# Optimization experiments

Hardware: AMD Instinct MI355X
Metric: run time of the kernel (lower is better)

The kernel has to match this reference:

```python
import jax, jax.numpy as jnp
import numpy as np

B, S, D, H = 2, 2048, 1024, 16
DK = D // H
NEG = -1e9
EPS = 1e-5


def setup_inputs() -> dict:
    key = jax.random.key(0)
    ks = jax.random.split(key, 6)
    sd = 0.02
    return {
        "x": jax.random.normal(ks[0], (B, S, D), jnp.float32),
        "mask": jax.random.randint(ks[1], (B, 1, S), 0, 2, jnp.int32),
        "wq": jax.random.normal(ks[2], (D, D), jnp.float32) * sd,
        "bq": jnp.zeros((D,), jnp.float32),
        "wk": jax.random.normal(ks[3], (D, D), jnp.float32) * sd,
        "bk": jnp.zeros((D,), jnp.float32),
        "wv": jax.random.normal(ks[4], (D, D), jnp.float32) * sd,
        "bv": jnp.zeros((D,), jnp.float32),
        "wf": jax.random.normal(ks[5], (D, D), jnp.float32) * sd,
        "bf": jnp.zeros((D,), jnp.float32),
        "ln_g": jnp.ones((D,), jnp.float32),
        "ln_b": jnp.zeros((D,), jnp.float32),
    }


def reference(x, mask, wq, bq, wk, bk, wv, bv, wf, bf, ln_g, ln_b):
    b, s, d = x.shape
    scale = jnp.asarray(DK ** 0.5, x.dtype)
    # QKV projections -> (b, h, s, dk)
    def split_heads(y):
        return y.reshape(b, s, H, DK).transpose(0, 2, 1, 3)
    q = split_heads(x @ wq + bq)
    k = split_heads(x @ wk + bk)
    v = split_heads(x @ wv + bv)
    # scores (b, h, s, s)
    att = jnp.einsum("bhqd,bhkd->bhqk", q / scale, k)
    m = mask[:, None, :, :]  # (b,1,1,s) broadcast over heads & queries
    att = jnp.where(m == 0, jnp.asarray(NEG, att.dtype), att)
    att = jax.nn.softmax(att, axis=-1)
    ctx = jnp.einsum("bhqk,bhkd->bhqd", att, v)
    ctx = ctx.transpose(0, 2, 1, 3).reshape(b, s, d)
    out = ctx @ wf + bf + x  # residual (dropout=0, eval)
    # LayerNorm
    mu = out.mean(-1, keepdims=True)
    var = out.var(-1, keepdims=True)
    out = (out - mu) * jax.lax.rsqrt(var + EPS) * ln_g + ln_b
    return out, att
```

## Files before the change

### kernel.cpp

```cpp
#include <hip/hip_runtime.h>

typedef unsigned short u16;
typedef unsigned int u32;
typedef unsigned long long u64;
typedef u16 u16x4 __attribute__((ext_vector_type(4)));
typedef u16 u16x8 __attribute__((ext_vector_type(8)));
typedef __bf16 bf16x8 __attribute__((ext_vector_type(8)));
typedef float f32x4 __attribute__((ext_vector_type(4)));

__device__ __forceinline__ u16 f2bf(float f) {
  u32 u = __float_as_uint(f);
  u += 0x7fffu + ((u >> 16) & 1u);
  return (u16)(u >> 16);
}

__device__ __forceinline__ f32x4 mfma16(bf16x8 a, bf16x8 b, f32x4 c) {
  return __builtin_amdgcn_mfma_f32_16x16x32_bf16(a, b, c, 0, 0, 0);
}

__device__ __forceinline__ void gload16(const void* g, void* l) {
  __builtin_amdgcn_global_load_lds(
      (const __attribute__((address_space(1))) unsigned char*)g,
      (__attribute__((address_space(3))) unsigned char*)l, 16, 0, 0);
}

__global__ __launch_bounds__(256) void cast_x_kernel(const float* __restrict__ x,
                                                     u16* __restrict__ xb) {
  int i = blockIdx.x * 256 + threadIdx.x;
  float4 v = ((const float4*)x)[i];
  u16x4 o = { f2bf(v.x), f2bf(v.y), f2bf(v.z), f2bf(v.w) };
  ((u16x4*)xb)[i] = o;
}

__global__ __launch_bounds__(256) void tcast_kernel(
    const float* __restrict__ w0, const float* __restrict__ w1,
    const float* __restrict__ w2, const float* __restrict__ w3,
    u16* __restrict__ o0, u16* __restrict__ o1, u16* __restrict__ o2, u16* __restrict__ o3) {
  const int z = blockIdx.z;
  const float* src = (z == 0) ? w0 : (z == 1) ? w1 : (z == 2) ? w2 : w3;
  u16* dst = (z == 0) ? o0 : (z == 1) ? o1 : (z == 2) ? o2 : o3;
  __shared__ u16 t[64][72];
  const int tid = threadIdx.x;
  const int n0 = blockIdx.x * 64, k0 = blockIdx.y * 64;
#pragma unroll
  for (int i = 0; i < 4; ++i) {
    int r = (tid >> 4) + i * 16;
    int c = (tid & 15) * 4;
    float4 v = *(const float4*)&src[(size_t)(k0 + r) * 1024 + n0 + c];
    t[c + 0][r] = f2bf(v.x);
    t[c + 1][r] = f2bf(v.y);
    t[c + 2][r] = f2bf(v.z);
    t[c + 3][r] = f2bf(v.w);
  }
  __syncthreads();
#pragma unroll
  for (int i = 0; i < 2; ++i) {
    int nl = (tid >> 3) + i * 32;
    int ks = (tid & 7) * 8;
    *(u16x8*)&dst[(size_t)(n0 + nl) * 1024 + k0 + ks] = *(const u16x8*)&t[nl][ks];
  }
}

__global__ __launch_bounds__(256, 2) void gemm_qkv_kernel(
    const u16* __restrict__ A,
    const u16* __restrict__ BqT, const u16* __restrict__ BkT, const u16* __restrict__ BvT,
    const float* __restrict__ bq, const float* __restrict__ bk, const float* __restrict__ bv,
    u16* __restrict__ qo, u16* __restrict__ ko, u16* __restrict__ vo) {
  const int z = blockIdx.z;
  const u16* Bt = (z == 0) ? BqT : (z == 1) ? BkT : BvT;
  const float* bias = (z == 0) ? bq : (z == 1) ? bk : bv;
  u16* outp = (z == 0) ? qo : (z == 1) ? ko : vo;
  const float osc = (z == 0) ? 0.125f : 1.0f;

  __shared__ u16 As[128][32];
  __shared__ u16 Bs[128][32];

  const int tid = threadIdx.x;
  const int lane = tid & 63, w = tid >> 6;
  const int wr = w >> 1, wc = w & 1;
  const int ln = lane & 15, quad = lane >> 4;
  const int kc = quad * 8;
  const int m0 = blockIdx.y * 128, n0 = blockIdx.x * 128;
  const int sr = w * 16 + (lane >> 2);
  const int sc = (lane & 3) * 8;

  f32x4 acc[4][4] = {};

  for (int k0 = 0; k0 < 1024; k0 += 32) {
    __syncthreads();
#pragma unroll
    for (int j = 0; j < 2; ++j) {
      gload16(&A[(size_t)(m0 + sr + j * 64) * 1024 + k0 + sc], &As[w * 16 + j * 64][0]);
      gload16(&Bt[(size_t)(n0 + sr + j * 64) * 1024 + k0 + sc], &Bs[w * 16 + j * 64][0]);
    }
    __syncthreads();
    bf16x8 af[4], bfr[4];
#pragma unroll
    for (int t = 0; t < 4; ++t) af[t] = *(const bf16x8*)&As[wr * 64 + t * 16 + ln][kc];
#pragma unroll
    for (int t = 0; t < 4; ++t) bfr[t] = *(const bf16x8*)&Bs[wc * 64 + t * 16 + ln][kc];
#pragma unroll
    for (int mt = 0; mt < 4; ++mt)
#pragma unroll
      for (int nt = 0; nt < 4; ++nt)
        acc[mt][nt] = mfma16(af[mt], bfr[nt], acc[mt][nt]);
  }

  if (z == 2) {
#pragma unroll
    for (int nt = 0; nt < 4; ++nt) {
      const int n = n0 + wc * 64 + nt * 16 + ln;
      const float bv2 = bias[n];
      const int h = n >> 6, dk = n & 63;
#pragma unroll
      for (int mt = 0; mt < 4; ++mt) {
        const int mb = m0 + wr * 64 + mt * 16 + quad * 4;
        const int b = mb >> 11, s = mb & 2047;
        u16x4 pk = { f2bf(acc[mt][nt][0] + bv2), f2bf(acc[mt][nt][1] + bv2),
                     f2bf(acc[mt][nt][2] + bv2), f2bf(acc[mt][nt][3] + bv2) };
        *(u16x4*)&outp[((size_t)((b * 16 + h) * 64 + dk)) * 2048 + s] = pk;
      }
    }
  } else {
#pragma unroll
    for (int nt = 0; nt < 4; ++nt) {
      const int n = n0 + wc * 64 + nt * 16 + ln;
      const float bv2 = bias[n];
      const int h = n >> 6, dk = n & 63;
#pragma unroll
      for (int mt = 0; mt < 4; ++mt) {
#pragma unroll
        for (int r = 0; r < 4; ++r) {
          const int m = m0 + wr * 64 + mt * 16 + quad * 4 + r;
          const int b = m >> 11, s = m & 2047;
          outp[((size_t)((b * 16 + h) * 2048 + s)) * 64 + dk] = f2bf((acc[mt][nt][r] + bv2) * osc);
        }
      }
    }
  }
}

__global__ __launch_bounds__(256, 3) void attn_kernel(
    const u16* __restrict__ q_ws, const u16* __restrict__ k_ws, const u16* __restrict__ vT,
    const int* __restrict__ mask, float* __restrict__ att, u16* __restrict__ ctx_ws) {
  __shared__ u16 Qs[64][72];
  __shared__ u16 KsF[2][64 * 64];
  __shared__ u16 VsF[2][64 * 64];
  __shared__ u16 PsF[4][16 * 64];

  const int tid = threadIdx.x, lane = tid & 63, w = tid >> 6;
  const int ln = lane & 15, quad = lane >> 4, kc = quad * 8;
  const int bh = blockIdx.y, b = bh >> 4, h = bh & 15;
  const int q0 = blockIdx.x * 64;
  const size_t base = (size_t)bh * 2048 * 64;
  const size_t vbase = (size_t)bh * 64 * 2048;

  const int rl = lane >> 3;
  const int sw16 = ((lane & 7) ^ rl) << 3;
  const int xi0 = (quad * 8) ^ ((ln & 7) << 3);
  const int xi1 = xi0 ^ 32;

  {
    int r = tid >> 2, c = (tid & 3) * 16;
    size_t g = base + (size_t)(q0 + r) * 64 + c;
    *(u16x8*)&Qs[r][c] = *(const u16x8*)&q_ws[g];
    *(u16x8*)&Qs[r][c + 8] = *(const u16x8*)&q_ws[g + 8];
  }

  const int* mrow = mask + b * 2048;
  u64 mm0 = 0, mm1 = 0;
#pragma unroll
  for (int kt = 0; kt < 16; ++kt) {
#pragma unroll
    for (int nt = 0; nt < 4; ++nt) {
      mm0 |= (u64)(mrow[kt * 64 + nt * 16 + ln] != 0) << (kt * 4 + nt);
      mm1 |= (u64)(mrow[(kt + 16) * 64 + nt * 16 + ln] != 0) << (kt * 4 + nt);
    }
  }

  {
    const int rr = w * 16;
    gload16(&k_ws[base + (size_t)(rr + rl) * 64 + sw16], &KsF[0][rr * 64]);
    gload16(&k_ws[base + (size_t)(rr + 8 + rl) * 64 + sw16], &KsF[0][(rr + 8) * 64]);
    gload16(&vT[vbase + (size_t)(rr + rl) * 2048 + sw16], &VsF[0][rr * 64]);
    gload16(&vT[vbase + (size_t)(rr + 8 + rl) * 2048 + sw16], &VsF[0][(rr + 8) * 64]);
  }
  __syncthreads();
  const bf16x8 aq0 = *(const bf16x8*)&Qs[w * 16 + ln][kc];
  const bf16x8 aq1 = *(const bf16x8*)&Qs[w * 16 + ln][kc + 32];

  float l_[4] = {0.f, 0.f, 0.f, 0.f};
  f32x4 ctx[4] = {};

  for (int kt = 0; kt < 32; ++kt) {
    const u16* Kc = KsF[kt & 1];
    const u16* Vc = VsF[kt & 1];
    if (kt < 31) {
      u16* Kn = KsF[(kt + 1) & 1];
      u16* Vn = VsF[(kt + 1) & 1];
      const int rr = w * 16;
#pragma unroll
      for (int j = 0; j < 2; ++j) {
        gload16(&k_ws[base + (size_t)((kt + 1) * 64 + rr + j * 8 + rl) * 64 + sw16],
                &Kn[(rr + j * 8) * 64]);
        gload16(&vT[vbase + (size_t)(rr + j * 8 + rl) * 2048 + (kt + 1) * 64 + sw16],
                &Vn[(rr + j * 8) * 64]);
      }
    }
    const u32 mbits = (u32)(((kt < 16) ? (mm0 >> ((kt & 15) * 4)) : (mm1 >> ((kt & 15) * 4))) & 0xf);
    f32x4 st[4];
#pragma unroll
    for (int nt = 0; nt < 4; ++nt) {
      const int row = nt * 16 + ln;
      bf16x8 b0 = *(const bf16x8*)&Kc[row * 64 + xi0];
      bf16x8 b1 = *(const bf16x8*)&Kc[row * 64 + xi1];
      f32x4 zz = {0.f, 0.f, 0.f, 0.f};
      zz = mfma16(aq0, b0, zz);
      zz = mfma16(aq1, b1, zz);
      st[nt] = zz;
    }
#pragma unroll
    for (int nt = 0; nt < 4; ++nt) {
      const float msel = (float)((mbits >> nt) & 1u);
#pragma unroll
      for (int r = 0; r < 4; ++r) {
        float p = __expf(st[nt][r]) * msel;
        st[nt][r] = p;
        const int qr = quad * 4 + r;
        PsF[w][(qr << 6) | ((nt * 16 + ln) ^ ((qr & 7) << 3))] = f2bf(p);
      }
    }
#pragma unroll
    for (int r = 0; r < 4; ++r) {
      float ss = st[0][r] + st[1][r] + st[2][r] + st[3][r];
      ss += __shfl_xor(ss, 1, 16);
      ss += __shfl_xor(ss, 2, 16);
      ss += __shfl_xor(ss, 4, 16);
      ss += __shfl_xor(ss, 8, 16);
      l_[r] += ss;
    }
    const int pr = ln * 64;
    const bf16x8 ap0 = *(const bf16x8*)&PsF[w][pr + xi0];
    const bf16x8 ap1 = *(const bf16x8*)&PsF[w][pr + xi1];
#pragma unroll
    for (int ct = 0; ct < 4; ++ct) {
      const int row = ct * 16 + ln;
      bf16x8 v0 = *(const bf16x8*)&Vc[row * 64 + xi0];
      bf16x8 v1 = *(const bf16x8*)&Vc[row * 64 + xi1];
      ctx[ct] = mfma16(ap0, v0, ctx[ct]);
      ctx[ct] = mfma16(ap1, v1, ctx[ct]);
    }
    __syncthreads();
  }

  float linv[4];
#pragma unroll
  for (int r = 0; r < 4; ++r) linv[r] = 1.0f / l_[r];
#pragma unroll
  for (int ct = 0; ct < 4; ++ct)
#pragma unroll
    for (int r = 0; r < 4; ++r) ctx[ct][r] *= linv[r];

#pragma unroll
  for (int ct = 0; ct < 4; ++ct) {
#pragma unroll
    for (int r = 0; r < 4; ++r) {
      int q = q0 + w * 16 + quad * 4 + r;
      int dk = ct * 16 + ln;
      ctx_ws[(size_t)(b * 2048 + q) * 1024 + h * 64 + dk] = f2bf(ctx[ct][r]);
    }
  }

  {
    const int rr = w * 16;
    gload16(&k_ws[base + (size_t)(rr + rl) * 64 + sw16], &KsF[0][rr * 64]);
    gload16(&k_ws[base + (size_t)(rr + 8 + rl) * 64 + sw16], &KsF[0][(rr + 8) * 64]);
  }
  __syncthreads();
  for (int kt = 0; kt < 32; ++kt) {
    const u16* Kc = KsF[kt & 1];
    if (kt < 31) {
      u16* Kn = KsF[(kt + 1) & 1];
      const int rr = w * 16;
#pragma unroll
      for (int j = 0; j < 2; ++j)
        gload16(&k_ws[base + (size_t)((kt + 1) * 64 + rr + j * 8 + rl) * 64 + sw16],
                &Kn[(rr + j * 8) * 64]);
    }
    const u32 mbits = (u32)(((kt < 16) ? (mm0 >> ((kt & 15) * 4)) : (mm1 >> ((kt & 15) * 4))) & 0xf);
    f32x4 st[4];
#pragma unroll
    for (int nt = 0; nt < 4; ++nt) {
      const int row = nt * 16 + ln;
      bf16x8 b0 = *(const bf16x8*)&Kc[row * 64 + xi0];
      bf16x8 b1 = *(const bf16x8*)&Kc[row * 64 + xi1];
      f32x4 zz = {0.f, 0.f, 0.f, 0.f};
      zz = mfma16(aq0, b0, zz);
      zz = mfma16(aq1, b1, zz);
      st[nt] = zz;
    }
#pragma unroll
    for (int nt = 0; nt < 4; ++nt) {
      const int sg = kt * 64 + nt * 16 + ln;
      const float msel = (float)((mbits >> nt) & 1u);
#pragma unroll
      for (int r = 0; r < 4; ++r) {
        float p = __expf(st[nt][r]) * linv[r] * msel;
        __builtin_nontemporal_store(
            p, &att[((size_t)bh * 2048 + q0 + w * 16 + quad * 4 + r) * 2048 + sg]);
      }
    }
    __syncthreads();
  }
}

__global__ __launch_bounds__(256, 2) void gemm_out_kernel(
    const u16* __restrict__ A, const u16* __restrict__ Bt, const float* __restrict__ bias,
    const float* __restrict__ resid, float* __restrict__ outp) {
  __shared__ u16 As[128][32];
  __shared__ u16 Bs[128][32];

  const int tid = threadIdx.x;
  const int lane = tid & 63, w = tid >> 6;
  const int wr = w >> 1, wc = w & 1;
  const int ln = lane & 15, quad = lane >> 4;
  const int kc = quad * 8;
  const int m0 = blockIdx.y * 128, n0 = blockIdx.x * 128;
  const int sr = w * 16 + (lane >> 2);
  const int sc = (lane & 3) * 8;

  f32x4 acc[4][4] = {};

  for (int k0 = 0; k0 < 1024; k0 += 32) {
    __syncthreads();
#pragma unroll
    for (int j = 0; j < 2; ++j) {
      gload16(&A[(size_t)(m0 + sr + j * 64) * 1024 + k0 + sc], &As[w * 16 + j * 64][0]);
      gload16(&Bt[(size_t)(n0 + sr + j * 64) * 1024 + k0 + sc], &Bs[w * 16 + j * 64][0]);
    }
    __syncthreads();
    bf16x8 af[4], bfr[4];
#pragma unroll
    for (int t = 0; t < 4; ++t) af[t] = *(const bf16x8*)&As[wr * 64 + t * 16 + ln][kc];
#pragma unroll
    for (int t = 0; t < 4; ++t) bfr[t] = *(const bf16x8*)&Bs[wc * 64 + t * 16 + ln][kc];
#pragma unroll
    for (int mt = 0; mt < 4; ++mt)
#pragma unroll
      for (int nt = 0; nt < 4; ++nt)
        acc[mt][nt] = mfma16(af[mt], bfr[nt], acc[mt][nt]);
  }

#pragma unroll
  for (int nt = 0; nt < 4; ++nt) {
    const int n = n0 + wc * 64 + nt * 16 + ln;
    const float bv2 = bias[n];
#pragma unroll
    for (int mt = 0; mt < 4; ++mt) {
#pragma unroll
      for (int r = 0; r < 4; ++r) {
        const int m = m0 + wr * 64 + mt * 16 + quad * 4 + r;
        outp[(size_t)m * 1024 + n] = acc[mt][nt][r] + bv2 + resid[(size_t)m * 1024 + n];
      }
    }
  }
}

__global__ __launch_bounds__(256) void ln_kernel(float* __restrict__ io,
                                                 const float* __restrict__ g,
                                                 const float* __restrict__ bta) {
  const int row = blockIdx.x, tid = threadIdx.x;
  float* p = io + (size_t)row * 1024;
  float4 v = ((const float4*)p)[tid];
  float s = v.x + v.y + v.z + v.w;
  float s2 = v.x * v.x + v.y * v.y + v.z * v.z + v.w * v.w;
#pragma unroll
  for (int off = 32; off > 0; off >>= 1) {
    s += __shfl_xor(s, off, 64);
    s2 += __shfl_xor(s2, off, 64);
  }
  __shared__ float red[8];
  const int w = tid >> 6, lane = tid & 63;
  if (lane == 0) { red[w] = s; red[4 + w] = s2; }
  __syncthreads();
  s = red[0] + red[1] + red[2] + red[3];
  s2 = red[4] + red[5] + red[6] + red[7];
  const float mu = s * (1.0f / 1024.0f);
  const float var = s2 * (1.0f / 1024.0f) - mu * mu;
  const float rs = rsqrtf(var + 1e-5f);
  float4 gg = ((const float4*)g)[tid];
  float4 bb = ((const float4*)bta)[tid];
  float4 o;
  o.x = (v.x - mu) * rs * gg.x + bb.x;
  o.y = (v.y - mu) * rs * gg.y + bb.y;
  o.z = (v.z - mu) * rs * gg.z + bb.z;
  o.w = (v.w - mu) * rs * gg.w + bb.w;
  ((float4*)p)[tid] = o;
}

extern "C" void kernel_launch(void* const* d_in, const int* in_sizes, int n_in,
                              void* d_out, int out_size, void* d_ws, size_t ws_size,
                              hipStream_t stream) {
  const float* x = (const float*)d_in[0];
  const int* mask = (const int*)d_in[1];
  const float* wq = (const float*)d_in[2];
  const float* bq = (const float*)d_in[3];
  const float* wk = (const float*)d_in[4];
  const float* bk = (const float*)d_in[5];
  const float* wv = (const float*)d_in[6];
  const float* bv = (const float*)d_in[7];
  const float* wf = (const float*)d_in[8];
  const float* bf_ = (const float*)d_in[9];
  const float* ln_g = (const float*)d_in[10];
  const float* ln_b = (const float*)d_in[11];

  float* out = (float*)d_out;
  float* att = out + (size_t)4194304;

  char* ws = (char*)d_ws;
  u16* xb   = (u16*)(ws);
  u16* wqT  = (u16*)(ws + ((size_t)8 << 20));
  u16* wkT  = (u16*)(ws + ((size_t)10 << 20));
  u16* wvT  = (u16*)(ws + ((size_t)12 << 20));
  u16* wfT  = (u16*)(ws + ((size_t)14 << 20));
  u16* q_ws = (u16*)(ws + ((size_t)16 << 20));
  u16* k_ws = (u16*)(ws + ((size_t)24 << 20));
  u16* vT   = (u16*)(ws + ((size_t)32 << 20));
  u16* ctxw = (u16*)(ws + ((size_t)40 << 20));

  cast_x_kernel<<<4096, 256, 0, stream>>>(x, xb);
  tcast_kernel<<<dim3(16, 16, 4), 256, 0, stream>>>(wq, wk, wv, wf, wqT, wkT, wvT, wfT);
  gemm_qkv_kernel<<<dim3(8, 32, 3), 256, 0, stream>>>(xb, wqT, wkT, wvT, bq, bk, bv,
                                                      q_ws, k_ws, vT);
  attn_kernel<<<dim3(32, 32), 256, 0, stream>>>(q_ws, k_ws, vT, mask, att, ctxw);
  gemm_out_kernel<<<dim3(8, 32), 256, 0, stream>>>(ctxw, wfT, bf_, x, out);
  ln_kernel<<<4096, 256, 0, stream>>>(out, ln_g, ln_b);
}
```

Baseline: 762.9 us.

## Split attention-probability store into separate kernel with vectorized transposed-MFMA writes

The second pass that recomputes QK^T and writes the full attention matrix moves out of the flash-attention kernel into its own kernel. The attention kernel now saves the per-row inverse softmax sums to a workspace buffer. The new kernel computes S^T with swapped MFMA operands, so each lane holds four consecutive keys and can issue 16-byte nontemporal float4 stores instead of scalar ones. The mask is staged as floats in LDS and Q is loaded directly into registers. The cost is an extra launch and reloading K, in exchange for coalesced writes of the 512 MB att output and lower register and LDS pressure in each kernel.

After: 836.4 us. 9.6% more time.

```diff
diff --git a/kernel.cpp b/kernel.cpp
--- a/kernel.cpp
+++ b/kernel.cpp
@@ -142,11 +142,11 @@
 
 __global__ __launch_bounds__(256, 3) void attn_kernel(
     const u16* __restrict__ q_ws, const u16* __restrict__ k_ws, const u16* __restrict__ vT,
-    const int* __restrict__ mask, float* __restrict__ att, u16* __restrict__ ctx_ws) {
-  __shared__ u16 Qs[64][72];
+    const int* __restrict__ mask, float* __restrict__ Lbuf, u16* __restrict__ ctx_ws) {
   __shared__ u16 KsF[2][64 * 64];
   __shared__ u16 VsF[2][64 * 64];
   __shared__ u16 PsF[4][16 * 64];
+  __shared__ float Ms[2048];
 
   const int tid = threadIdx.x, lane = tid & 63, w = tid >> 6;
   const int ln = lane & 15, quad = lane >> 4, kc = quad * 8;
@@ -161,22 +161,17 @@
   const int xi1 = xi0 ^ 32;
 
   {
-    int r = tid >> 2, c = (tid & 3) * 16;
-    size_t g = base + (size_t)(q0 + r) * 64 + c;
-    *(u16x8*)&Qs[r][c] = *(const u16x8*)&q_ws[g];
-    *(u16x8*)&Qs[r][c + 8] = *(const u16x8*)&q_ws[g + 8];
-  }
-
-  const int* mrow = mask + b * 2048;
-  u64 mm0 = 0, mm1 = 0;
-#pragma unroll
-  for (int kt = 0; kt < 16; ++kt) {
-#pragma unroll
-    for (int nt = 0; nt < 4; ++nt) {
-      mm0 |= (u64)(mrow[kt * 64 + nt * 16 + ln] != 0) << (kt * 4 + nt);
-      mm1 |= (u64)(mrow[(kt + 16) * 64 + nt * 16 + ln] != 0) << (kt * 4 + nt);
-    }
-  }
+    const int* mrow = mask + b * 2048;
+    int4 a0 = ((const int4*)mrow)[tid * 2];
+    int4 a1 = ((const int4*)mrow)[tid * 2 + 1];
+    float4 f0 = { a0.x ? 1.f : 0.f, a0.y ? 1.f : 0.f, a0.z ? 1.f : 0.f, a0.w ? 1.f : 0.f };
+    float4 f1 = { a1.x ? 1.f : 0.f, a1.y ? 1.f : 0.f, a1.z ? 1.f : 0.f, a1.w ? 1.f : 0.f };
+    *(float4*)&Ms[tid * 8] = f0;
+    *(float4*)&Ms[tid * 8 + 4] = f1;
+  }
+
+  const bf16x8 aq0 = *(const bf16x8*)&q_ws[base + (size_t)(q0 + w * 16 + ln) * 64 + kc];
+  const bf16x8 aq1 = *(const bf16x8*)&q_ws[base + (size_t)(q0 + w * 16 + ln) * 64 + kc + 32];
 
   {
     const int rr = w * 16;
@@ -186,8 +181,6 @@
     gload16(&vT[vbase + (size_t)(rr + 8 + rl) * 2048 + sw16], &VsF[0][(rr + 8) * 64]);
   }
   __syncthreads();
-  const bf16x8 aq0 = *(const bf16x8*)&Qs[w * 16 + ln][kc];
-  const bf16x8 aq1 = *(const bf16x8*)&Qs[w * 16 + ln][kc + 32];
 
   float l_[4] = {0.f, 0.f, 0.f, 0.f};
   f32x4 ctx[4] = {};
@@ -207,7 +200,6 @@
                 &Vn[(rr + j * 8) * 64]);
       }
     }
-    const u32 mbits = (u32)(((kt < 16) ? (mm0 >> ((kt & 15) * 4)) : (mm1 >> ((kt & 15) * 4))) & 0xf);
     f32x4 st[4];
 #pragma unroll
     for (int nt = 0; nt < 4; ++nt) {
@@ -221,7 +213,7 @@
     }
 #pragma unroll
     for (int nt = 0; nt < 4; ++nt) {
-      const float msel = (float)((mbits >> nt) & 1u);
+      const float msel = Ms[kt * 64 + nt * 16 + ln];
 #pragma unroll
       for (int r = 0; r < 4; ++r) {
         float p = __expf(st[nt][r]) * msel;
@@ -261,6 +253,11 @@
 #pragma unroll
     for (int r = 0; r < 4; ++r) ctx[ct][r] *= linv[r];
 
+  if (ln == 0) {
+#pragma unroll
+    for (int r = 0; r < 4; ++r) Lbuf[(size_t)bh * 2048 + q0 + w * 16 + quad * 4 + r] = linv[r];
+  }
+
 #pragma unroll
   for (int ct = 0; ct < 4; ++ct) {
 #pragma unroll
@@ -270,6 +267,40 @@
       ctx_ws[(size_t)(b * 2048 + q) * 1024 + h * 64 + dk] = f2bf(ctx[ct][r]);
     }
   }
+}
+
+__global__ __launch_bounds__(256, 4) void att_store_kernel(
+    const u16* __restrict__ q_ws, const u16* __restrict__ k_ws,
+    const int* __restrict__ mask, const float* __restrict__ Lbuf,
+    float* __restrict__ att) {
+  __shared__ u16 KsF[2][64 * 64];
+  __shared__ float Ms[2048];
+
+  const int tid = threadIdx.x, lane = tid & 63, w = tid >> 6;
+  const int ln = lane & 15, quad = lane >> 4, kc = quad * 8;
+  const int bh = blockIdx.y, b = bh >> 4;
+  const int q0 = blockIdx.x * 64;
+  const size_t base = (size_t)bh * 2048 * 64;
+
+  const int rl = lane >> 3;
+  const int sw16 = ((lane & 7) ^ rl) << 3;
+  const int xi0 = (quad * 8) ^ ((ln & 7) << 3);
+  const int xi1 = xi0 ^ 32;
+
+  {
+    const int* mrow = mask + b * 2048;
+    int4 a0 = ((const int4*)mrow)[tid * 2];
+    int4 a1 = ((const int4*)mrow)[tid * 2 + 1];
+    float4 f0 = { a0.x ? 1.f : 0.f, a0.y ? 1.f : 0.f, a0.z ? 1.f : 0.f, a0.w ? 1.f : 0.f };
+    float4 f1 = { a1.x ? 1.f : 0.f, a1.y ? 1.f : 0.f, a1.z ? 1.f : 0.f, a1.w ? 1.f : 0.f };
+    *(float4*)&Ms[tid * 8] = f0;
+    *(float4*)&Ms[tid * 8 + 4] = f1;
+  }
+
+  const bf16x8 aq0 = *(const bf16x8*)&q_ws[base + (size_t)(q0 + w * 16 + ln) * 64 + kc];
+  const bf16x8 aq1 = *(const bf16x8*)&q_ws[base + (size_t)(q0 + w * 16 + ln) * 64 + kc + 32];
+  const float lsv = Lbuf[(size_t)bh * 2048 + q0 + w * 16 + ln];
+  float* orow = att + ((size_t)bh * 2048 + q0 + w * 16 + ln) * 2048;
 
   {
     const int rr = w * 16;
@@ -277,6 +308,7 @@
     gload16(&k_ws[base + (size_t)(rr + 8 + rl) * 64 + sw16], &KsF[0][(rr + 8) * 64]);
   }
   __syncthreads();
+
   for (int kt = 0; kt < 32; ++kt) {
     const u16* Kc = KsF[kt & 1];
     if (kt < 31) {
@@ -287,28 +319,21 @@
         gload16(&k_ws[base + (size_t)((kt + 1) * 64 + rr + j * 8 + rl) * 64 + sw16],
                 &Kn[(rr + j * 8) * 64]);
     }
-    const u32 mbits = (u32)(((kt < 16) ? (mm0 >> ((kt & 15) * 4)) : (mm1 >> ((kt & 15) * 4))) & 0xf);
-    f32x4 st[4];
 #pragma unroll
     for (int nt = 0; nt < 4; ++nt) {
       const int row = nt * 16 + ln;
       bf16x8 b0 = *(const bf16x8*)&Kc[row * 64 + xi0];
       bf16x8 b1 = *(const bf16x8*)&Kc[row * 64 + xi1];
       f32x4 zz = {0.f, 0.f, 0.f, 0.f};
-      zz = mfma16(aq0, b0, zz);
-      zz = mfma16(aq1, b1, zz);
-      st[nt] = zz;
-    }
-#pragma unroll
-    for (int nt = 0; nt < 4; ++nt) {
-      const int sg = kt * 64 + nt * 16 + ln;
-      const float msel = (float)((mbits >> nt) & 1u);
-#pragma unroll
-      for (int r = 0; r < 4; ++r) {
-        float p = __expf(st[nt][r]) * linv[r] * msel;
-        __builtin_nontemporal_store(
-            p, &att[((size_t)bh * 2048 + q0 + w * 16 + quad * 4 + r) * 2048 + sg]);
-      }
+      zz = mfma16(b0, aq0, zz);
+      zz = mfma16(b1, aq1, zz);
+      const float4 msk = *(const float4*)&Ms[kt * 64 + nt * 16 + quad * 4];
+      f32x4 o;
+      o[0] = __expf(zz[0]) * lsv * msk.x;
+      o[1] = __expf(zz[1]) * lsv * msk.y;
+      o[2] = __expf(zz[2]) * lsv * msk.z;
+      o[3] = __expf(zz[3]) * lsv * msk.w;
+      __builtin_nontemporal_store(o, (f32x4*)&orow[kt * 64 + nt * 16 + quad * 4]);
     }
     __syncthreads();
   }
@@ -427,12 +452,14 @@
   u16* k_ws = (u16*)(ws + ((size_t)24 << 20));
   u16* vT   = (u16*)(ws + ((size_t)32 << 20));
   u16* ctxw = (u16*)(ws + ((size_t)40 << 20));
+  float* Lbuf = (float*)ws;
 
   cast_x_kernel<<<4096, 256, 0, stream>>>(x, xb);
   tcast_kernel<<<dim3(16, 16, 4), 256, 0, stream>>>(wq, wk, wv, wf, wqT, wkT, wvT, wfT);
   gemm_qkv_kernel<<<dim3(8, 32, 3), 256, 0, stream>>>(xb, wqT, wkT, wvT, bq, bk, bv,
                                                       q_ws, k_ws, vT);
-  attn_kernel<<<dim3(32, 32), 256, 0, stream>>>(q_ws, k_ws, vT, mask, att, ctxw);
+  attn_kernel<<<dim3(32, 32), 256, 0, stream>>>(q_ws, k_ws, vT, mask, Lbuf, ctxw);
+  att_store_kernel<<<dim3(32, 32), 256, 0, stream>>>(q_ws, k_ws, mask, Lbuf, att);
   gemm_out_kernel<<<dim3(8, 32), 256, 0, stream>>>(ctxw, wfT, bf_, x, out);
   ln_kernel<<<4096, 256, 0, stream>>>(out, ln_g, ln_b);
 }
```
